# Performance work log

Measured on AMD Instinct MI355X. Metric: run time of the kernel, lower is better.

## Reference

```python
import jax, jax.numpy as jnp
import numpy as np

NW = 30000      # num_words (word nodes)
ND = 8192       # num_docs
D = 300         # hidden_dim
D2 = D // 2
NNZ_A = 600000  # nnz of word-word adjacency A_norm [NW, NW]
NNZ_X = 524288  # nnz of doc-word tfidf X [ND, NW]
ALPHA = 0.7     # residual_alpha
LN_EPS = 1e-5
BN_SCALE = float(1.0 / np.sqrt(1.0 + 1e-5))  # eval BN, running_mean=0, running_var=1


def _xavier(k, shape):
    fan_out, fan_in = shape[0], shape[1]
    lim = float(np.sqrt(6.0 / (fan_in + fan_out)))
    return jax.random.uniform(k, shape, jnp.float32, -lim, lim)


def setup_inputs() -> dict:
    key = jax.random.key(0)
    ks = jax.random.split(key, 13)
    return {
        "a_rows": jax.random.randint(ks[0], (NNZ_A,), 0, NW, dtype=jnp.int32),
        "a_cols": jax.random.randint(ks[1], (NNZ_A,), 0, NW, dtype=jnp.int32),
        "a_vals": jax.random.uniform(ks[2], (NNZ_A,), jnp.float32) * 0.05,
        "x_rows": jax.random.randint(ks[3], (NNZ_X,), 0, ND, dtype=jnp.int32),
        "x_cols": jax.random.randint(ks[4], (NNZ_X,), 0, NW, dtype=jnp.int32),
        "x_vals": jax.random.uniform(ks[5], (NNZ_X,), jnp.float32) * 0.05,
        "emb": _xavier(ks[6], (NW, D)),
        "w1": _xavier(ks[7], (D, D)),
        "w2": _xavier(ks[8], (D, D)),
        "w3": _xavier(ks[9], (D, D)),
        "ln_g": jnp.ones((D,), jnp.float32),
        "ln_b": jnp.zeros((D,), jnp.float32),
        "m_w1": _xavier(ks[10], (D, D)),
        "m_b1": jnp.zeros((D,), jnp.float32),
        "bn1_g": jnp.ones((D,), jnp.float32),
        "bn1_b": jnp.zeros((D,), jnp.float32),
        "m_w2": _xavier(ks[11], (D2, D)),
        "m_b2": jnp.zeros((D2,), jnp.float32),
        "bn2_g": jnp.ones((D2,), jnp.float32),
        "bn2_b": jnp.zeros((D2,), jnp.float32),
        "clf_w": _xavier(ks[12], (2, D2)),
        "clf_b": jnp.zeros((2,), jnp.float32),
    }


def _spmm(rows, cols, vals, H, n):
    # sparse [n, m] @ dense [m, d] via gather + segment-sum (COO SpMM)
    return jax.ops.segment_sum(vals[:, None] * H[cols], rows, num_segments=n)


def _layernorm(x, g, b):
    mu = jnp.mean(x, axis=-1, keepdims=True)
    var = jnp.var(x, axis=-1, keepdims=True)
    return (x - mu) * jax.lax.rsqrt(var + LN_EPS) * g + b


def _bn_eval(x, g, b):
    # BatchNorm1d in eval mode with freshly-initialized running stats (mean=0, var=1)
    return x * (g * BN_SCALE) + b


def reference(a_rows, a_cols, a_vals, x_rows, x_cols, x_vals, emb, w1, w2, w3,
              ln_g, ln_b, m_w1, m_b1, bn1_g, bn1_b, m_w2, m_b2, bn2_g, bn2_b,
              clf_w, clf_b):
    H0 = emb
    H = jax.nn.relu(_spmm(a_rows, a_cols, a_vals, H0, NW) @ w1.T)
    H = jax.nn.relu(_spmm(a_rows, a_cols, a_vals, H, NW) @ w2.T)
    H = jax.nn.relu(_spmm(a_rows, a_cols, a_vals, H, NW) @ w3.T)
    H = (1.0 - ALPHA) * H0 + ALPHA * H
    word_H = _layernorm(H, ln_g, ln_b)
    # --- doc aggregation: X_tfidf @ word_H + X_tfidf @ emb ---
    doc_H = (_spmm(x_rows, x_cols, x_vals, word_H, ND)
             + _spmm(x_rows, x_cols, x_vals, emb, ND))
    # --- MLP head (dropout inactive in eval) ---
    h = jax.nn.relu(_bn_eval(doc_H @ m_w1.T + m_b1, bn1_g, bn1_b))
    h = jax.nn.relu(_bn_eval(h @ m_w2.T + m_b2, bn2_g, bn2_b))
    return h @ clf_w.T + clf_b  # [ND, 2]
```

## Files before the change

### kernel.cpp

```cpp
#include <hip/hip_runtime.h>

#define NW 30000
#define ND 8192
#define DIM 300
#define DIM2 150
#define NNZA 600000
#define NNZX 524288
#define PD 320
#define PD_U 160
#define BN_SCALE 0.99999500003749971f

typedef unsigned int uint;
typedef unsigned short ushort;
typedef __attribute__((ext_vector_type(8))) short bf16x8;
typedef __attribute__((ext_vector_type(4))) float f32x4;

static inline int cdiv(int a, int b){ return (a + b - 1) / b; }

__device__ __forceinline__ float b2f_lo(uint u){ return __builtin_bit_cast(float, u << 16); }
__device__ __forceinline__ float b2f_hi(uint u){ return __builtin_bit_cast(float, u & 0xffff0000u); }
__device__ __forceinline__ ushort f2b(float f){
  uint u = __builtin_bit_cast(uint, f);
  u += 0x7fffu + ((u >> 16) & 1u);
  return (ushort)(u >> 16);
}
__device__ __forceinline__ uint packb(float x, float y){
  return (uint)f2b(x) | ((uint)f2b(y) << 16);
}

__global__ void k_hist(const int* __restrict__ rows, int n, int* __restrict__ cnt){
  int i = blockIdx.x * blockDim.x + threadIdx.x;
  if (i < n) atomicAdd(&cnt[rows[i]], 1);
}

__global__ void k_copy_int(const int* __restrict__ a, int* __restrict__ b, int n){
  int i = blockIdx.x * blockDim.x + threadIdx.x;
  if (i < n) b[i] = a[i];
}

__global__ __launch_bounds__(1024) void k_scan(const int* __restrict__ cnt, int n, int* __restrict__ rp){
  __shared__ int sd[1024];
  __shared__ int carry;
  const int t = threadIdx.x;
  if (t == 0) carry = 0;
  __syncthreads();
  int nch = (n + 1023) >> 10;
  for (int c = 0; c < nch; ++c){
    int i = (c << 10) + t;
    int v = (i < n) ? cnt[i] : 0;
    sd[t] = v;
    __syncthreads();
    for (int o = 1; o < 1024; o <<= 1){
      int x = (t >= o) ? sd[t - o] : 0;
      __syncthreads();
      sd[t] += x;
      __syncthreads();
    }
    if (i < n) rp[i] = carry + sd[t] - v;
    __syncthreads();
    if (t == 1023) carry += sd[1023];
    __syncthreads();
  }
  if (t == 0) rp[n] = carry;
}

__global__ void k_scatter(const int* __restrict__ rows, const int* __restrict__ cols,
                          const float* __restrict__ vals, int n, int* __restrict__ cursor,
                          int* __restrict__ cs, float* __restrict__ vs){
  int i = blockIdx.x * blockDim.x + threadIdx.x;
  if (i < n){
    int r = rows[i];
    int p = atomicAdd(&cursor[r], 1);
    cs[p] = cols[i];
    vs[p] = vals[i];
  }
}

__global__ void k_f2b_pad(const float* __restrict__ src, ushort* __restrict__ dst,
                          int srows, int scols, int dstride){
  int r = blockIdx.y;
  int c = blockIdx.x * blockDim.x + threadIdx.x;
  if (c >= dstride) return;
  ushort v = 0;
  if (r < srows && c < scols) v = f2b(src[(size_t)r * scols + c]);
  dst[(size_t)r * dstride + c] = v;
}

__global__ __launch_bounds__(256) void k_spmm_b(const int* __restrict__ rp, const int* __restrict__ cs,
        const float* __restrict__ vs, const uint* __restrict__ Hb, uint* __restrict__ Ob, int nrows){
  int wid = (blockIdx.x * blockDim.x + threadIdx.x) >> 6;
  int lane = threadIdx.x & 63;
  if (wid >= nrows) return;
  int s = rp[wid], e = rp[wid + 1];
  const bool half = lane < 32;
  float a0=0,a1=0,a2=0,a3=0,a4=0,a5=0;
  float c0_=0,c1_=0,c2_=0,c3_=0,c4_=0,c5_=0;
  int k = s;
  for (; k + 2 <= e; k += 2){
    int i0 = cs[k], i1 = cs[k+1];
    float v0 = vs[k], v1 = vs[k+1];
    const uint* p0 = Hb + (size_t)i0 * PD_U;
    const uint* p1 = Hb + (size_t)i1 * PD_U;
    uint u0 = p0[lane], u1 = p0[lane + 64];
    uint w0 = p1[lane], w1 = p1[lane + 64];
    uint u2 = 0, w2 = 0;
    if (half){ u2 = p0[lane + 128]; w2 = p1[lane + 128]; }
    a0 = fmaf(v0, b2f_lo(u0), a0); a1 = fmaf(v0, b2f_hi(u0), a1);
    a2 = fmaf(v0, b2f_lo(u1), a2); a3 = fmaf(v0, b2f_hi(u1), a3);
    a4 = fmaf(v0, b2f_lo(u2), a4); a5 = fmaf(v0, b2f_hi(u2), a5);
    c0_ = fmaf(v1, b2f_lo(w0), c0_); c1_ = fmaf(v1, b2f_hi(w0), c1_);
    c2_ = fmaf(v1, b2f_lo(w1), c2_); c3_ = fmaf(v1, b2f_hi(w1), c3_);
    c4_ = fmaf(v1, b2f_lo(w2), c4_); c5_ = fmaf(v1, b2f_hi(w2), c5_);
  }
  if (k < e){
    int i0 = cs[k];
    float v0 = vs[k];
    const uint* p0 = Hb + (size_t)i0 * PD_U;
    uint u0 = p0[lane], u1 = p0[lane + 64];
    uint u2 = half ? p0[lane + 128] : 0;
    a0 = fmaf(v0, b2f_lo(u0), a0); a1 = fmaf(v0, b2f_hi(u0), a1);
    a2 = fmaf(v0, b2f_lo(u1), a2); a3 = fmaf(v0, b2f_hi(u1), a3);
    a4 = fmaf(v0, b2f_lo(u2), a4); a5 = fmaf(v0, b2f_hi(u2), a5);
  }
  a0+=c0_; a1+=c1_; a2+=c2_; a3+=c3_; a4+=c4_; a5+=c5_;
  uint* o = Ob + (size_t)wid * PD_U;
  o[lane] = packb(a0, a1);
  o[lane + 64] = packb(a2, a3);
  if (half) o[lane + 128] = packb(a4, a5);
}

__global__ __launch_bounds__(256) void k_mgemm(const ushort* __restrict__ A, const ushort* __restrict__ B,
        const float* __restrict__ bias, const float* __restrict__ bng, const float* __restrict__ bnb,
        ushort* __restrict__ C, int M, int Nvalid, int ldc, int relu){
  __shared__ ushort As[128][72];
  __shared__ ushort Bs[160][72];
  const int t = threadIdx.x;
  const int wid = t >> 6, lane = t & 63;
  const int bm = blockIdx.y << 7;
  const int bn = blockIdx.x * 160;
  const int wm = (wid >> 1) << 6;
  const int wn = (wid & 1) * 80;
  const int r16 = lane & 15;
  const int h8 = (lane >> 4) << 3;
  f32x4 acc[4][5] = {};
  for (int k0 = 0; k0 < PD; k0 += 64){
    #pragma unroll
    for (int i = 0; i < 4; ++i){
      int q = t + (i << 8);
      int r = q >> 3, c = (q & 7) << 3;
      int gm = bm + r; if (gm >= M) gm = M - 1;
      *(bf16x8*)(&As[r][c]) = *(const bf16x8*)(A + (size_t)gm * PD + k0 + c);
    }
    #pragma unroll
    for (int i = 0; i < 5; ++i){
      int q = t + (i << 8);
      int r = q >> 3, c = (q & 7) << 3;
      *(bf16x8*)(&Bs[r][c]) = *(const bf16x8*)(B + (size_t)(bn + r) * PD + k0 + c);
    }
    __syncthreads();
    #pragma unroll
    for (int kk = 0; kk < 2; ++kk){
      bf16x8 af[4], bfr[5];
      #pragma unroll
      for (int m = 0; m < 4; ++m)
        af[m] = *(const bf16x8*)(&As[wm + m * 16 + r16][kk * 32 + h8]);
      #pragma unroll
      for (int n = 0; n < 5; ++n)
        bfr[n] = *(const bf16x8*)(&Bs[wn + n * 16 + r16][kk * 32 + h8]);
      #pragma unroll
      for (int m = 0; m < 4; ++m)
        #pragma unroll
        for (int n = 0; n < 5; ++n)
          acc[m][n] = __builtin_amdgcn_mfma_f32_16x16x32_bf16(af[m], bfr[n], acc[m][n], 0, 0, 0);
    }
    __syncthreads();
  }
  const int cr = (lane >> 4) << 2;
  #pragma unroll
  for (int m = 0; m < 4; ++m){
    #pragma unroll
    for (int n = 0; n < 5; ++n){
      int col = bn + wn + n * 16 + r16;
      #pragma unroll
      for (int j = 0; j < 4; ++j){
        int row = bm + wm + m * 16 + cr + j;
        if (row >= M) continue;
        float v = acc[m][n][j];
        if (col < Nvalid){
          if (bias) v += bias[col];
          if (bng)  v = v * (bng[col] * BN_SCALE) + bnb[col];
          if (relu) v = fmaxf(v, 0.f);
        } else v = 0.f;
        C[(size_t)row * ldc + col] = f2b(v);
      }
    }
  }
}

__global__ __launch_bounds__(64) void k_res_ln(const float* __restrict__ emb, const uint* __restrict__ Hb,
        const float* __restrict__ g, const float* __restrict__ bb, uint* __restrict__ S){
  int row = blockIdx.x, lane = threadIdx.x;
  const float* e = emb + (size_t)row * DIM;
  const uint* h = Hb + (size_t)row * PD_U;
  float x[6], ev[6];
  float sum = 0.f, sq = 0.f;
  #pragma unroll
  for (int j = 0; j < 3; ++j){
    int i = lane + j * 64;
    float e0 = 0.f, e1 = 0.f, h0 = 0.f, h1 = 0.f;
    if (i < 150){
      uint u = h[i];
      h0 = b2f_lo(u); h1 = b2f_hi(u);
      e0 = e[2 * i]; e1 = e[2 * i + 1];
    }
    float v0 = 0.3f * e0 + 0.7f * h0;
    float v1 = 0.3f * e1 + 0.7f * h1;
    if (i >= 150){ v0 = 0.f; v1 = 0.f; }
    x[2*j] = v0; x[2*j+1] = v1; ev[2*j] = e0; ev[2*j+1] = e1;
    sum += v0 + v1; sq += v0 * v0 + v1 * v1;
  }
  #pragma unroll
  for (int o = 32; o > 0; o >>= 1){ sum += __shfl_down(sum, o); sq += __shfl_down(sq, o); }
  sum = __shfl(sum, 0); sq = __shfl(sq, 0);
  const float inv = 1.f / (float)DIM;
  float mu = sum * inv;
  float var = sq * inv - mu * mu;
  float rs = rsqrtf(var + 1e-5f);
  uint* o = S + (size_t)row * PD_U;
  #pragma unroll
  for (int j = 0; j < 3; ++j){
    int i = lane + j * 64;
    if (i >= PD_U) continue;
    uint w = 0;
    if (i < 150){
      float r0 = (x[2*j]   - mu) * rs * g[2*i]   + bb[2*i]   + ev[2*j];
      float r1 = (x[2*j+1] - mu) * rs * g[2*i+1] + bb[2*i+1] + ev[2*j+1];
      w = packb(r0, r1);
    }
    o[i] = w;
  }
}

__global__ void k_clf(const uint* __restrict__ h2, const float* __restrict__ w,
                      const float* __restrict__ bias, float* __restrict__ out){
  int m = blockIdx.x * blockDim.x + threadIdx.x;
  if (m >= ND) return;
  const uint* hr = h2 + (size_t)m * 80;
  float s0 = bias[0], s1 = bias[1];
  #pragma unroll 5
  for (int i = 0; i < 75; ++i){
    uint u = hr[i];
    float h0 = b2f_lo(u), h1 = b2f_hi(u);
    int k = 2 * i;
    s0 = fmaf(h0, w[k], fmaf(h1, w[k + 1], s0));
    s1 = fmaf(h0, w[DIM2 + k], fmaf(h1, w[DIM2 + k + 1], s1));
  }
  out[m * 2] = s0;
  out[m * 2 + 1] = s1;
}

extern "C" void kernel_launch(void* const* d_in, const int* in_sizes, int n_in,
                              void* d_out, int out_size, void* d_ws, size_t ws_size,
                              hipStream_t stream){
  const int*   a_rows = (const int*)  d_in[0];
  const int*   a_cols = (const int*)  d_in[1];
  const float* a_vals = (const float*)d_in[2];
  const int*   x_rows = (const int*)  d_in[3];
  const int*   x_cols = (const int*)  d_in[4];
  const float* x_vals = (const float*)d_in[5];
  const float* emb    = (const float*)d_in[6];
  const float* w1     = (const float*)d_in[7];
  const float* w2     = (const float*)d_in[8];
  const float* w3     = (const float*)d_in[9];
  const float* ln_g   = (const float*)d_in[10];
  const float* ln_b   = (const float*)d_in[11];
  const float* m_w1   = (const float*)d_in[12];
  const float* m_b1   = (const float*)d_in[13];
  const float* bn1_g  = (const float*)d_in[14];
  const float* bn1_b  = (const float*)d_in[15];
  const float* m_w2   = (const float*)d_in[16];
  const float* m_b2   = (const float*)d_in[17];
  const float* bn2_g  = (const float*)d_in[18];
  const float* bn2_b  = (const float*)d_in[19];
  const float* clf_w  = (const float*)d_in[20];
  const float* clf_b  = (const float*)d_in[21];
  float* out = (float*)d_out;

  char* ws = (char*)d_ws;
  size_t off = 0;
  auto take = [&](size_t nbytes)->void*{
    void* p = ws + off;
    off += (nbytes + 255) & ~(size_t)255;
    return p;
  };
  int*    a_rp   = (int*)   take((NW + 1) * 4);
  int*    a_cs   = (int*)   take((size_t)NNZA * 4);
  float*  a_vs   = (float*) take((size_t)NNZA * 4);
  int*    x_rp   = (int*)   take((ND + 1) * 4);
  int*    x_cs   = (int*)   take((size_t)NNZX * 4);
  float*  x_vs   = (float*) take((size_t)NNZX * 4);
  int*    cursor = (int*)   take((size_t)NW * 4);
  ushort* embb   = (ushort*)take((size_t)NW * PD * 2);
  ushort* Tb     = (ushort*)take((size_t)NW * PD * 2);
  ushort* Hb     = (ushort*)take((size_t)NW * PD * 2);
  ushort* w1b    = (ushort*)take((size_t)PD * PD * 2);
  ushort* w2b    = (ushort*)take((size_t)PD * PD * 2);
  ushort* w3b    = (ushort*)take((size_t)PD * PD * 2);
  ushort* mw1b   = (ushort*)take((size_t)PD * PD * 2);
  ushort* mw2b   = (ushort*)take((size_t)PD * PD * 2);
  ushort* docHb = Hb;
  ushort* h1b   = Hb + (size_t)ND * PD;
  ushort* h2b   = Hb + (size_t)2 * ND * PD;

  hipMemsetAsync(cursor, 0, NW * 4, stream);
  k_hist<<<cdiv(NNZA, 256), 256, 0, stream>>>(a_rows, NNZA, cursor);
  k_scan<<<1, 1024, 0, stream>>>(cursor, NW, a_rp);
  k_copy_int<<<cdiv(NW, 256), 256, 0, stream>>>(a_rp, cursor, NW);
  k_scatter<<<cdiv(NNZA, 256), 256, 0, stream>>>(a_rows, a_cols, a_vals, NNZA, cursor, a_cs, a_vs);
  hipMemsetAsync(cursor, 0, ND * 4, stream);
  k_hist<<<cdiv(NNZX, 256), 256, 0, stream>>>(x_rows, NNZX, cursor);
  k_scan<<<1, 1024, 0, stream>>>(cursor, ND, x_rp);
  k_copy_int<<<cdiv(ND, 256), 256, 0, stream>>>(x_rp, cursor, ND);
  k_scatter<<<cdiv(NNZX, 256), 256, 0, stream>>>(x_rows, x_cols, x_vals, NNZX, cursor, x_cs, x_vs);

  dim3 cb(cdiv(PD, 256), NW);
  k_f2b_pad<<<cb, 256, 0, stream>>>(emb, embb, NW, DIM, PD);
  dim3 cw(cdiv(PD, 256), PD);
  k_f2b_pad<<<cw, 256, 0, stream>>>(w1, w1b, DIM, DIM, PD);
  k_f2b_pad<<<cw, 256, 0, stream>>>(w2, w2b, DIM, DIM, PD);
  k_f2b_pad<<<cw, 256, 0, stream>>>(w3, w3b, DIM, DIM, PD);
  k_f2b_pad<<<cw, 256, 0, stream>>>(m_w1, mw1b, DIM, DIM, PD);
  k_f2b_pad<<<cw, 256, 0, stream>>>(m_w2, mw2b, DIM2, DIM, PD);

  dim3 gg(2, cdiv(NW, 128));
  k_spmm_b<<<cdiv(NW, 4), 256, 0, stream>>>(a_rp, a_cs, a_vs, (const uint*)embb, (uint*)Tb, NW);
  k_mgemm<<<gg, 256, 0, stream>>>(Tb, w1b, nullptr, nullptr, nullptr, Hb, NW, DIM, PD, 1);
  k_spmm_b<<<cdiv(NW, 4), 256, 0, stream>>>(a_rp, a_cs, a_vs, (const uint*)Hb, (uint*)Tb, NW);
  k_mgemm<<<gg, 256, 0, stream>>>(Tb, w2b, nullptr, nullptr, nullptr, Hb, NW, DIM, PD, 1);
  k_spmm_b<<<cdiv(NW, 4), 256, 0, stream>>>(a_rp, a_cs, a_vs, (const uint*)Hb, (uint*)Tb, NW);
  k_mgemm<<<gg, 256, 0, stream>>>(Tb, w3b, nullptr, nullptr, nullptr, Hb, NW, DIM, PD, 1);
  k_res_ln<<<NW, 64, 0, stream>>>(emb, (const uint*)Hb, ln_g, ln_b, (uint*)Tb);
  k_spmm_b<<<cdiv(ND, 4), 256, 0, stream>>>(x_rp, x_cs, x_vs, (const uint*)Tb, (uint*)docHb, ND);
  dim3 g1(2, cdiv(ND, 128));
  k_mgemm<<<g1, 256, 0, stream>>>(docHb, mw1b, m_b1, bn1_g, bn1_b, h1b, ND, DIM, PD, 1);
  dim3 g2(1, cdiv(ND, 128));
  k_mgemm<<<g2, 256, 0, stream>>>(h1b, mw2b, m_b2, bn2_g, bn2_b, h2b, ND, DIM2, 160, 1);
  k_clf<<<cdiv(ND, 256), 256, 0, stream>>>((const uint*)h2b, clf_w, clf_b, out);
}
```

Measured before the change: 602.0 us.

## Parallelize CSR scan, vectorize bf16 conversion, unroll SpMM gather by four

```diff
diff --git a/kernel.cpp b/kernel.cpp
--- a/kernel.cpp
+++ b/kernel.cpp
@@ -14,6 +14,7 @@
 typedef unsigned short ushort;
 typedef __attribute__((ext_vector_type(8))) short bf16x8;
 typedef __attribute__((ext_vector_type(4))) float f32x4;
+typedef __attribute__((ext_vector_type(4))) uint uint4v;
 
 static inline int cdiv(int a, int b){ return (a + b - 1) / b; }
 
@@ -38,30 +39,49 @@
   if (i < n) b[i] = a[i];
 }
 
-__global__ __launch_bounds__(1024) void k_scan(const int* __restrict__ cnt, int n, int* __restrict__ rp){
+__global__ __launch_bounds__(1024) void k_bsum(const int* __restrict__ cnt, int n, int* __restrict__ bs){
   __shared__ int sd[1024];
-  __shared__ int carry;
-  const int t = threadIdx.x;
-  if (t == 0) carry = 0;
+  int t = threadIdx.x;
+  int i = blockIdx.x * 1024 + t;
+  sd[t] = (i < n) ? cnt[i] : 0;
   __syncthreads();
-  int nch = (n + 1023) >> 10;
-  for (int c = 0; c < nch; ++c){
-    int i = (c << 10) + t;
-    int v = (i < n) ? cnt[i] : 0;
-    sd[t] = v;
-    __syncthreads();
-    for (int o = 1; o < 1024; o <<= 1){
-      int x = (t >= o) ? sd[t - o] : 0;
-      __syncthreads();
-      sd[t] += x;
-      __syncthreads();
-    }
-    if (i < n) rp[i] = carry + sd[t] - v;
-    __syncthreads();
-    if (t == 1023) carry += sd[1023];
-    __syncthreads();
-  }
-  if (t == 0) rp[n] = carry;
+  #pragma unroll
+  for (int o = 512; o > 0; o >>= 1){
+    if (t < o) sd[t] += sd[t + o];
+    __syncthreads();
+  }
+  if (t == 0) bs[blockIdx.x] = sd[0];
+}
+
+__global__ __launch_bounds__(64) void k_scan_small(int* __restrict__ bs, int nb,
+                                                   int* __restrict__ rp, int n){
+  int t = threadIdx.x;
+  int orig = (t < nb) ? bs[t] : 0;
+  int v = orig;
+  #pragma unroll
+  for (int o = 1; o < 64; o <<= 1){
+    int x = __shfl_up(v, o);
+    if (t >= o) v += x;
+  }
+  if (t < nb) bs[t] = v - orig;
+  if (t == nb - 1) rp[n] = v;
+}
+
+__global__ __launch_bounds__(1024) void k_scan_apply(const int* __restrict__ cnt, int n,
+        const int* __restrict__ bs, int* __restrict__ rp){
+  __shared__ int sd[1024];
+  int t = threadIdx.x;
+  int i = blockIdx.x * 1024 + t;
+  int v = (i < n) ? cnt[i] : 0;
+  sd[t] = v;
+  __syncthreads();
+  for (int o = 1; o < 1024; o <<= 1){
+    int x = (t >= o) ? sd[t - o] : 0;
+    __syncthreads();
+    sd[t] += x;
+    __syncthreads();
+  }
+  if (i < n) rp[i] = bs[blockIdx.x] + sd[t] - v;
 }
 
 __global__ void k_scatter(const int* __restrict__ rows, const int* __restrict__ cols,
@@ -76,14 +96,21 @@
   }
 }
 
-__global__ void k_f2b_pad(const float* __restrict__ src, ushort* __restrict__ dst,
-                          int srows, int scols, int dstride){
-  int r = blockIdx.y;
-  int c = blockIdx.x * blockDim.x + threadIdx.x;
-  if (c >= dstride) return;
-  ushort v = 0;
-  if (r < srows && c < scols) v = f2b(src[(size_t)r * scols + c]);
-  dst[(size_t)r * dstride + c] = v;
+__global__ void k_f2b_pad8(const float* __restrict__ src, ushort* __restrict__ dst,
+                           int srows, int scols, int drows, int dstride){
+  int q = blockIdx.x * blockDim.x + threadIdx.x;
+  int perRow = dstride >> 3;
+  int r = q / perRow;
+  int c = (q - r * perRow) << 3;
+  if (r >= drows) return;
+  float x[8];
+  #pragma unroll
+  for (int j = 0; j < 8; ++j)
+    x[j] = (r < srows && c + j < scols) ? src[(size_t)r * scols + c + j] : 0.f;
+  uint4v o;
+  o.x = packb(x[0], x[1]); o.y = packb(x[2], x[3]);
+  o.z = packb(x[4], x[5]); o.w = packb(x[6], x[7]);
+  *(uint4v*)(dst + (size_t)r * dstride + c) = o;
 }
 
 __global__ __launch_bounds__(256) void k_spmm_b(const int* __restrict__ rp, const int* __restrict__ cs,
@@ -93,40 +120,44 @@
   if (wid >= nrows) return;
   int s = rp[wid], e = rp[wid + 1];
   const bool half = lane < 32;
-  float a0=0,a1=0,a2=0,a3=0,a4=0,a5=0;
-  float c0_=0,c1_=0,c2_=0,c3_=0,c4_=0,c5_=0;
+  float acc[4][6] = {};
   int k = s;
-  for (; k + 2 <= e; k += 2){
-    int i0 = cs[k], i1 = cs[k+1];
-    float v0 = vs[k], v1 = vs[k+1];
-    const uint* p0 = Hb + (size_t)i0 * PD_U;
-    const uint* p1 = Hb + (size_t)i1 * PD_U;
-    uint u0 = p0[lane], u1 = p0[lane + 64];
-    uint w0 = p1[lane], w1 = p1[lane + 64];
-    uint u2 = 0, w2 = 0;
-    if (half){ u2 = p0[lane + 128]; w2 = p1[lane + 128]; }
-    a0 = fmaf(v0, b2f_lo(u0), a0); a1 = fmaf(v0, b2f_hi(u0), a1);
-    a2 = fmaf(v0, b2f_lo(u1), a2); a3 = fmaf(v0, b2f_hi(u1), a3);
-    a4 = fmaf(v0, b2f_lo(u2), a4); a5 = fmaf(v0, b2f_hi(u2), a5);
-    c0_ = fmaf(v1, b2f_lo(w0), c0_); c1_ = fmaf(v1, b2f_hi(w0), c1_);
-    c2_ = fmaf(v1, b2f_lo(w1), c2_); c3_ = fmaf(v1, b2f_hi(w1), c3_);
-    c4_ = fmaf(v1, b2f_lo(w2), c4_); c5_ = fmaf(v1, b2f_hi(w2), c5_);
-  }
-  if (k < e){
-    int i0 = cs[k];
-    float v0 = vs[k];
-    const uint* p0 = Hb + (size_t)i0 * PD_U;
-    uint u0 = p0[lane], u1 = p0[lane + 64];
-    uint u2 = half ? p0[lane + 128] : 0;
-    a0 = fmaf(v0, b2f_lo(u0), a0); a1 = fmaf(v0, b2f_hi(u0), a1);
-    a2 = fmaf(v0, b2f_lo(u1), a2); a3 = fmaf(v0, b2f_hi(u1), a3);
-    a4 = fmaf(v0, b2f_lo(u2), a4); a5 = fmaf(v0, b2f_hi(u2), a5);
-  }
-  a0+=c0_; a1+=c1_; a2+=c2_; a3+=c3_; a4+=c4_; a5+=c5_;
+  for (; k + 4 <= e; k += 4){
+    #pragma unroll
+    for (int j = 0; j < 4; ++j){
+      int c = cs[k + j];
+      float v = vs[k + j];
+      const uint* p = Hb + (size_t)c * PD_U;
+      uint u0 = p[lane], u1 = p[lane + 64];
+      uint u2 = half ? p[lane + 128] : 0;
+      acc[j][0] = fmaf(v, b2f_lo(u0), acc[j][0]);
+      acc[j][1] = fmaf(v, b2f_hi(u0), acc[j][1]);
+      acc[j][2] = fmaf(v, b2f_lo(u1), acc[j][2]);
+      acc[j][3] = fmaf(v, b2f_hi(u1), acc[j][3]);
+      acc[j][4] = fmaf(v, b2f_lo(u2), acc[j][4]);
+      acc[j][5] = fmaf(v, b2f_hi(u2), acc[j][5]);
+    }
+  }
+  for (; k < e; ++k){
+    int c = cs[k];
+    float v = vs[k];
+    const uint* p = Hb + (size_t)c * PD_U;
+    uint u0 = p[lane], u1 = p[lane + 64];
+    uint u2 = half ? p[lane + 128] : 0;
+    acc[0][0] = fmaf(v, b2f_lo(u0), acc[0][0]);
+    acc[0][1] = fmaf(v, b2f_hi(u0), acc[0][1]);
+    acc[0][2] = fmaf(v, b2f_lo(u1), acc[0][2]);
+    acc[0][3] = fmaf(v, b2f_hi(u1), acc[0][3]);
+    acc[0][4] = fmaf(v, b2f_lo(u2), acc[0][4]);
+    acc[0][5] = fmaf(v, b2f_hi(u2), acc[0][5]);
+  }
+  #pragma unroll
+  for (int d = 0; d < 6; ++d)
+    acc[0][d] += (acc[1][d] + acc[2][d]) + acc[3][d];
   uint* o = Ob + (size_t)wid * PD_U;
-  o[lane] = packb(a0, a1);
-  o[lane + 64] = packb(a2, a3);
-  if (half) o[lane + 128] = packb(a4, a5);
+  o[lane] = packb(acc[0][0], acc[0][1]);
+  o[lane + 64] = packb(acc[0][2], acc[0][3]);
+  if (half) o[lane + 128] = packb(acc[0][4], acc[0][5]);
 }
 
 __global__ __launch_bounds__(256) void k_mgemm(const ushort* __restrict__ A, const ushort* __restrict__ B,
@@ -300,6 +331,7 @@
   int*    x_cs   = (int*)   take((size_t)NNZX * 4);
   float*  x_vs   = (float*) take((size_t)NNZX * 4);
   int*    cursor = (int*)   take((size_t)NW * 4);
+  int*    bsums  = (int*)   take(64 * 4);
   ushort* embb   = (ushort*)take((size_t)NW * PD * 2);
   ushort* Tb     = (ushort*)take((size_t)NW * PD * 2);
   ushort* Hb     = (ushort*)take((size_t)NW * PD * 2);
@@ -312,25 +344,29 @@
   ushort* h1b   = Hb + (size_t)ND * PD;
   ushort* h2b   = Hb + (size_t)2 * ND * PD;
 
+  int nbA = cdiv(NW, 1024);
   hipMemsetAsync(cursor, 0, NW * 4, stream);
   k_hist<<<cdiv(NNZA, 256), 256, 0, stream>>>(a_rows, NNZA, cursor);
-  k_scan<<<1, 1024, 0, stream>>>(cursor, NW, a_rp);
+  k_bsum<<<nbA, 1024, 0, stream>>>(cursor, NW, bsums);
+  k_scan_small<<<1, 64, 0, stream>>>(bsums, nbA, a_rp, NW);
+  k_scan_apply<<<nbA, 1024, 0, stream>>>(cursor, NW, bsums, a_rp);
   k_copy_int<<<cdiv(NW, 256), 256, 0, stream>>>(a_rp, cursor, NW);
   k_scatter<<<cdiv(NNZA, 256), 256, 0, stream>>>(a_rows, a_cols, a_vals, NNZA, cursor, a_cs, a_vs);
+  int nbX = cdiv(ND, 1024);
   hipMemsetAsync(cursor, 0, ND * 4, stream);
   k_hist<<<cdiv(NNZX, 256), 256, 0, stream>>>(x_rows, NNZX, cursor);
-  k_scan<<<1, 1024, 0, stream>>>(cursor, ND, x_rp);
+  k_bsum<<<nbX, 1024, 0, stream>>>(cursor, ND, bsums);
+  k_scan_small<<<1, 64, 0, stream>>>(bsums, nbX, x_rp, ND);
+  k_scan_apply<<<nbX, 1024, 0, stream>>>(cursor, ND, bsums, x_rp);
   k_copy_int<<<cdiv(ND, 256), 256, 0, stream>>>(x_rp, cursor, ND);
   k_scatter<<<cdiv(NNZX, 256), 256, 0, stream>>>(x_rows, x_cols, x_vals, NNZX, cursor, x_cs, x_vs);
 
-  dim3 cb(cdiv(PD, 256), NW);
-  k_f2b_pad<<<cb, 256, 0, stream>>>(emb, embb, NW, DIM, PD);
-  dim3 cw(cdiv(PD, 256), PD);
-  k_f2b_pad<<<cw, 256, 0, stream>>>(w1, w1b, DIM, DIM, PD);
-  k_f2b_pad<<<cw, 256, 0, stream>>>(w2, w2b, DIM, DIM, PD);
-  k_f2b_pad<<<cw, 256, 0, stream>>>(w3, w3b, DIM, DIM, PD);
-  k_f2b_pad<<<cw, 256, 0, stream>>>(m_w1, mw1b, DIM, DIM, PD);
-  k_f2b_pad<<<cw, 256, 0, stream>>>(m_w2, mw2b, DIM2, DIM, PD);
+  k_f2b_pad8<<<cdiv(NW * 40, 256), 256, 0, stream>>>(emb, embb, NW, DIM, NW, PD);
+  k_f2b_pad8<<<cdiv(PD * 40, 256), 256, 0, stream>>>(w1, w1b, DIM, DIM, PD, PD);
+  k_f2b_pad8<<<cdiv(PD * 40, 256), 256, 0, stream>>>(w2, w2b, DIM, DIM, PD, PD);
+  k_f2b_pad8<<<cdiv(PD * 40, 256), 256, 0, stream>>>(w3, w3b, DIM, DIM, PD, PD);
+  k_f2b_pad8<<<cdiv(PD * 40, 256), 256, 0, stream>>>(m_w1, mw1b, DIM, DIM, PD, PD);
+  k_f2b_pad8<<<cdiv(PD * 40, 256), 256, 0, stream>>>(m_w2, mw2b, DIM2, DIM, PD, PD);
 
   dim3 gg(2, cdiv(NW, 128));
   k_spmm_b<<<cdiv(NW, 4), 256, 0, stream>>>(a_rp, a_cs, a_vs, (const uint*)embb, (uint*)Tb, NW);
```

Result: faster. 557.9 us (-7.3%).
